# Kernel optimization log

Hardware: AMD Instinct MI355X
Metric: run time of the kernel (lower is better)

Reference implementation:

```python
import jax, jax.numpy as jnp
import numpy as np

K = 8        # fused SOS sections
C = 64       # channels (B*C after reshape)
T = 262144   # time samples (~6 s @ 44.1 kHz)


def setup_inputs() -> dict:
    key = jax.random.key(0)
    kx, kb, ka1, ka2 = jax.random.split(key, 4)
    x = jax.random.normal(kx, (C, T), dtype=jnp.float32)
    # Stable biquad coefficients: a0 = 1, |a1| < 0.5, |a2| < 0.4 keeps poles
    # strictly inside the unit circle (|a1| < 1 + a2 and |a2| < 1).
    b = jax.random.normal(kb, (K, 3), dtype=jnp.float32) * 0.3
    a1 = jax.random.uniform(ka1, (K, 1), minval=-0.5, maxval=0.5, dtype=jnp.float32)
    a2 = jax.random.uniform(ka2, (K, 1), minval=-0.4, maxval=0.4, dtype=jnp.float32)
    sos = jnp.concatenate([b, jnp.ones((K, 1), jnp.float32), a1, a2], axis=1)
    state_x = jnp.zeros((K, C, 2), jnp.float32)  # [x[n-1], x[n-2]] per section/channel
    state_y = jnp.zeros((K, C, 2), jnp.float32)  # [y[n-1], y[n-2]]
    return {"x": x, "sos": sos, "state_x": state_x, "state_y": state_y}


def _biquad_df1(x, b0, b1, b2, a1, a2, sx, sy):
    """Direct-form-1 biquad over time, vectorized across channels.

    x: [C, T]; sx, sy: [C, 2] holding (lag1, lag2). Returns y: [C, T].
    """
    def step(carry, xn):
        x1, x2, y1, y2 = carry
        yn = b0 * xn + b1 * x1 + b2 * x2 - a1 * y1 - a2 * y2
        return (xn, x1, yn, y1), yn

    init = (sx[:, 0], sx[:, 1], sy[:, 0], sy[:, 1])
    _, ys = jax.lax.scan(step, init, x.T)  # scan over T, carry [C]
    return ys.T


def reference(x, sos, state_x, state_y):
    # Serial cascade of K second-order sections (fallback path of forward()).
    out = x
    k = sos.shape[0]
    for s in range(k):
        out = _biquad_df1(out, sos[s, 0], sos[s, 1], sos[s, 2],
                          sos[s, 4], sos[s, 5], state_x[s], state_y[s])
    return out
```

## Files before the change

kernel.cpp:

```cpp
#include <hip/hip_runtime.h>

#define C 64
#define T 262144
#define K 8
#define L 128
#define W 192
#define B (T / L)
#define TT 64
#define STRIDE 65

__device__ __forceinline__ void async_ld(const float* gp, float* ldsbase) {
  __builtin_amdgcn_global_load_lds(
      (const __attribute__((address_space(1))) void*)gp,
      (__attribute__((address_space(3))) void*)ldsbase, 4, 0, 0);
}

#define STEP(Y1, Y2, U1, U2, XIN)                                            \
  {                                                                          \
    float tkv[K];                                                            \
    tkv[0] = fmaf(b1c[0], U1,                                                \
             fmaf(b2c[0], U2, fmaf(na1[0], Y1[0], na2[0] * Y2[0])));         \
    _Pragma("unroll")                                                        \
    for (int k = 1; k < K; ++k)                                              \
      tkv[k] = fmaf(b1c[k], Y1[k - 1],                                       \
               fmaf(b2c[k], Y2[k - 1],                                       \
               fmaf(na1[k], Y1[k], na2[k] * Y2[k])));                        \
    float o = fmaf(b0c[0], (XIN), tkv[0]);                                   \
    U2 = (XIN);                                                              \
    _Pragma("unroll")                                                        \
    for (int k = 1; k < K; ++k) {                                            \
      float o2 = fmaf(b0c[k], o, tkv[k]);                                    \
      Y2[k - 1] = o;                                                         \
      o = o2;                                                                \
    }                                                                        \
    Y2[K - 1] = o;                                                           \
    lastout = o;                                                             \
  }

__global__ __launch_bounds__(64) void sos_kernel(
    const float* __restrict__ x, const float* __restrict__ sos,
    const float* __restrict__ sx, const float* __restrict__ sy,
    float* __restrict__ out) {
  __shared__ float lbuf[64 * STRIDE];

  const int h = blockIdx.x;
  const int b = (h & 7) * (B / 8) + (h >> 3);
  const int lane = threadIdx.x;

  float b0c[K], b1c[K], b2c[K], na1[K], na2[K];
#pragma unroll
  for (int k = 0; k < K; ++k) {
    b0c[k] = sos[k * 6 + 0];
    b1c[k] = sos[k * 6 + 1];
    b2c[k] = sos[k * 6 + 2];
    na1[k] = -sos[k * 6 + 4];
    na2[k] = -sos[k * 6 + 5];
  }

  const int t_out = b * L;
  const int tstart = (t_out >= W) ? (t_out - W) : 0;
  const int nch = (t_out + L - tstart) / TT;

  float yA[K], yB[K], uA, uB;
  if (tstart == 0) {
    uA = sx[lane * 2 + 0];
    uB = sx[lane * 2 + 1];
#pragma unroll
    for (int k = 0; k < K; ++k) {
      yA[k] = sy[(k * 64 + lane) * 2 + 0];
      yB[k] = sy[(k * 64 + lane) * 2 + 1];
    }
  } else {
    uA = x[(size_t)lane * T + tstart - 1];
    uB = x[(size_t)lane * T + tstart - 2];
#pragma unroll
    for (int k = 0; k < K; ++k) { yA[k] = 0.f; yB[k] = 0.f; }
  }

  float lastout = 0.f;
  for (int ch = 0; ch < nch; ++ch) {
    const int tc = tstart + ch * TT;
    __syncthreads();
#pragma unroll
    for (int r = 0; r < 64; ++r)
      async_ld(x + (size_t)r * T + tc + lane, &lbuf[r * STRIDE]);
    __syncthreads();

    float* myrow = &lbuf[lane * STRIDE];

    float xg0[8], xg1[8];
#pragma unroll
    for (int j = 0; j < 8; ++j) xg0[j] = myrow[j];
    for (int gg = 0; gg < TT / 16; ++gg) {
      const int tb = gg * 16;
#pragma unroll
      for (int j = 0; j < 8; ++j) xg1[j] = myrow[tb + 8 + j];
#pragma unroll
      for (int j = 0; j < 8; j += 2) {
        STEP(yA, yB, uA, uB, xg0[j])
        myrow[tb + j] = lastout;
        STEP(yB, yA, uB, uA, xg0[j + 1])
        myrow[tb + j + 1] = lastout;
      }
      if (gg + 1 < TT / 16) {
#pragma unroll
        for (int j = 0; j < 8; ++j) xg0[j] = myrow[tb + 16 + j];
      }
#pragma unroll
      for (int j = 0; j < 8; j += 2) {
        STEP(yA, yB, uA, uB, xg1[j])
        myrow[tb + 8 + j] = lastout;
        STEP(yB, yA, uB, uA, xg1[j + 1])
        myrow[tb + 8 + j + 1] = lastout;
      }
    }

    if (tc >= t_out) {
      __syncthreads();
#pragma unroll 8
      for (int r = 0; r < 64; ++r)
        out[(size_t)r * T + tc + lane] = lbuf[r * STRIDE + lane];
    }
  }
  (void)lastout;
}

extern "C" void kernel_launch(void* const* d_in, const int* in_sizes, int n_in,
                              void* d_out, int out_size, void* d_ws,
                              size_t ws_size, hipStream_t stream) {
  const float* x = (const float*)d_in[0];
  const float* sos = (const float*)d_in[1];
  const float* sx = (const float*)d_in[2];
  const float* sy = (const float*)d_in[3];
  float* out = (float*)d_out;
  (void)d_ws;

  sos_kernel<<<B, 64, 0, stream>>>(x, sos, sx, sy, out);
}
```

Measured before the change: 160.6 us.

## Prefetch next chunk into registers during compute and vectorize output stores

Replaces the direct global-to-LDS async loads with register staging: each lane loads the next 64-sample chunk into a 64-float register array while the current chunk is filtered, then writes it into LDS after the compute. The aim is to hide global load latency behind the recurrence instead of stalling at a barrier before each chunk. Output stores become float4 writes over a remapped lane/row layout, and launch bounds ask for 2 blocks per CU. The 64-register staging buffer adds register pressure, which may cause spills or lower occupancy.

```diff
diff --git a/kernel.cpp b/kernel.cpp
--- a/kernel.cpp
+++ b/kernel.cpp
@@ -8,12 +8,6 @@
 #define B (T / L)
 #define TT 64
 #define STRIDE 65
-
-__device__ __forceinline__ void async_ld(const float* gp, float* ldsbase) {
-  __builtin_amdgcn_global_load_lds(
-      (const __attribute__((address_space(1))) void*)gp,
-      (__attribute__((address_space(3))) void*)ldsbase, 4, 0, 0);
-}
 
 #define STEP(Y1, Y2, U1, U2, XIN)                                            \
   {                                                                          \
@@ -37,7 +31,7 @@
     lastout = o;                                                             \
   }
 
-__global__ __launch_bounds__(64) void sos_kernel(
+__global__ __launch_bounds__(64, 2) void sos_kernel(
     const float* __restrict__ x, const float* __restrict__ sos,
     const float* __restrict__ sx, const float* __restrict__ sy,
     float* __restrict__ out) {
@@ -77,14 +71,23 @@
     for (int k = 0; k < K; ++k) { yA[k] = 0.f; yB[k] = 0.f; }
   }
 
+  float st[64];
+
+#pragma unroll
+  for (int r = 0; r < 64; ++r) st[r] = x[(size_t)r * T + tstart + lane];
+#pragma unroll
+  for (int r = 0; r < 64; ++r) lbuf[r * STRIDE + lane] = st[r];
+  __syncthreads();
+
   float lastout = 0.f;
   for (int ch = 0; ch < nch; ++ch) {
     const int tc = tstart + ch * TT;
-    __syncthreads();
+
+    if (ch + 1 < nch) {
+      const int tn = tc + TT;
 #pragma unroll
-    for (int r = 0; r < 64; ++r)
-      async_ld(x + (size_t)r * T + tc + lane, &lbuf[r * STRIDE]);
-    __syncthreads();
+      for (int r = 0; r < 64; ++r) st[r] = x[(size_t)r * T + tn + lane];
+    }
 
     float* myrow = &lbuf[lane * STRIDE];
 
@@ -115,11 +118,28 @@
       }
     }
 
+    __syncthreads();
+
     if (tc >= t_out) {
+      const int rr = lane >> 4;
+      const int cc = (lane & 15) * 4;
+#pragma unroll
+      for (int it = 0; it < 16; ++it) {
+        const int r = it * 4 + rr;
+        float4 v;
+        v.x = lbuf[r * STRIDE + cc + 0];
+        v.y = lbuf[r * STRIDE + cc + 1];
+        v.z = lbuf[r * STRIDE + cc + 2];
+        v.w = lbuf[r * STRIDE + cc + 3];
+        *reinterpret_cast<float4*>(&out[(size_t)r * T + tc + cc]) = v;
+      }
+      if (ch + 1 < nch) __syncthreads();
+    }
+
+    if (ch + 1 < nch) {
+#pragma unroll
+      for (int r = 0; r < 64; ++r) lbuf[r * STRIDE + lane] = st[r];
       __syncthreads();
-#pragma unroll 8
-      for (int r = 0; r < 64; ++r)
-        out[(size_t)r * T + tc + lane] = lbuf[r * STRIDE + lane];
     }
   }
   (void)lastout;
```

Result: no change. 159.6 us (-0.6%).

## Load input straight into registers with prefetch instead of LDS staging

Applied to the files above, without the earlier changes.

Drops the per-chunk async global-to-LDS transpose of the input, along with its two barriers. Each lane now reads its own channel row as float4 vectors into two 16-element register buffers, and the next group is prefetched while the current one is filtered. Output is still staged through LDS, but it is written to global memory with coalesced float4 stores, and the launch bound now requests two blocks per SIMD. In exchange, the per-lane global loads are strided across rows, register pressure goes up, and the barrier before the output transpose is gone, which relies on the block being a single wavefront.

```diff
diff --git a/kernel.cpp b/kernel.cpp
--- a/kernel.cpp
+++ b/kernel.cpp
@@ -7,13 +7,8 @@
 #define W 192
 #define B (T / L)
 #define TT 64
-#define STRIDE 65
-
-__device__ __forceinline__ void async_ld(const float* gp, float* ldsbase) {
-  __builtin_amdgcn_global_load_lds(
-      (const __attribute__((address_space(1))) void*)gp,
-      (__attribute__((address_space(3))) void*)ldsbase, 4, 0, 0);
-}
+#define OSTRIDE 65
+#define TMAX (T - 16)
 
 #define STEP(Y1, Y2, U1, U2, XIN)                                            \
   {                                                                          \
@@ -37,11 +32,30 @@
     lastout = o;                                                             \
   }
 
-__global__ __launch_bounds__(64) void sos_kernel(
+#define GROUP(XS, CBASE)                                                     \
+  _Pragma("unroll")                                                          \
+  for (int j = 0; j < 16; j += 2) {                                          \
+    STEP(yA, yB, uA, uB, XS[j])                                              \
+    orow[(CBASE) + j] = lastout;                                             \
+    STEP(yB, yA, uB, uA, XS[j + 1])                                          \
+    orow[(CBASE) + j + 1] = lastout;                                         \
+  }
+
+#define LOAD16(DST, PTR)                                                     \
+  {                                                                          \
+    const float4* p4_ = (const float4*)(PTR);                                \
+    float4 q0_ = p4_[0], q1_ = p4_[1], q2_ = p4_[2], q3_ = p4_[3];           \
+    DST[0] = q0_.x;  DST[1] = q0_.y;  DST[2] = q0_.z;  DST[3] = q0_.w;       \
+    DST[4] = q1_.x;  DST[5] = q1_.y;  DST[6] = q1_.z;  DST[7] = q1_.w;       \
+    DST[8] = q2_.x;  DST[9] = q2_.y;  DST[10] = q2_.z; DST[11] = q2_.w;      \
+    DST[12] = q3_.x; DST[13] = q3_.y; DST[14] = q3_.z; DST[15] = q3_.w;      \
+  }
+
+__global__ __launch_bounds__(64, 2) void sos_kernel(
     const float* __restrict__ x, const float* __restrict__ sos,
     const float* __restrict__ sx, const float* __restrict__ sy,
     float* __restrict__ out) {
-  __shared__ float lbuf[64 * STRIDE];
+  __shared__ float obuf[64 * OSTRIDE];
 
   const int h = blockIdx.x;
   const int b = (h & 7) * (B / 8) + (h >> 3);
@@ -61,6 +75,9 @@
   const int tstart = (t_out >= W) ? (t_out - W) : 0;
   const int nch = (t_out + L - tstart) / TT;
 
+  const float* xrow = x + (size_t)lane * T;
+  float* orow = &obuf[lane * OSTRIDE];
+
   float yA[K], yB[K], uA, uB;
   if (tstart == 0) {
     uA = sx[lane * 2 + 0];
@@ -71,55 +88,44 @@
       yB[k] = sy[(k * 64 + lane) * 2 + 1];
     }
   } else {
-    uA = x[(size_t)lane * T + tstart - 1];
-    uB = x[(size_t)lane * T + tstart - 2];
+    uA = xrow[tstart - 1];
+    uB = xrow[tstart - 2];
 #pragma unroll
     for (int k = 0; k < K; ++k) { yA[k] = 0.f; yB[k] = 0.f; }
   }
 
+  float xA[16], xB[16];
+  LOAD16(xA, xrow + tstart)
+  LOAD16(xB, xrow + tstart + 16)
+
   float lastout = 0.f;
   for (int ch = 0; ch < nch; ++ch) {
     const int tc = tstart + ch * TT;
-    __syncthreads();
-#pragma unroll
-    for (int r = 0; r < 64; ++r)
-      async_ld(x + (size_t)r * T + tc + lane, &lbuf[r * STRIDE]);
-    __syncthreads();
 
-    float* myrow = &lbuf[lane * STRIDE];
-
-    float xg0[8], xg1[8];
-#pragma unroll
-    for (int j = 0; j < 8; ++j) xg0[j] = myrow[j];
-    for (int gg = 0; gg < TT / 16; ++gg) {
-      const int tb = gg * 16;
-#pragma unroll
-      for (int j = 0; j < 8; ++j) xg1[j] = myrow[tb + 8 + j];
-#pragma unroll
-      for (int j = 0; j < 8; j += 2) {
-        STEP(yA, yB, uA, uB, xg0[j])
-        myrow[tb + j] = lastout;
-        STEP(yB, yA, uB, uA, xg0[j + 1])
-        myrow[tb + j + 1] = lastout;
-      }
-      if (gg + 1 < TT / 16) {
-#pragma unroll
-        for (int j = 0; j < 8; ++j) xg0[j] = myrow[tb + 16 + j];
-      }
-#pragma unroll
-      for (int j = 0; j < 8; j += 2) {
-        STEP(yA, yB, uA, uB, xg1[j])
-        myrow[tb + 8 + j] = lastout;
-        STEP(yB, yA, uB, uA, xg1[j + 1])
-        myrow[tb + 8 + j + 1] = lastout;
-      }
-    }
+    GROUP(xA, 0)
+    { int tl = tc + 32;  LOAD16(xA, xrow + tl) }
+    GROUP(xB, 16)
+    { int tl = tc + 48;  LOAD16(xB, xrow + tl) }
+    GROUP(xA, 32)
+    { int tl = tc + 64;  if (tl > TMAX) tl = TMAX;
+      LOAD16(xA, xrow + tl) }
+    GROUP(xB, 48)
+    { int tl = tc + 80;  if (tl > TMAX) tl = TMAX;
+      LOAD16(xB, xrow + tl) }
 
     if (tc >= t_out) {
-      __syncthreads();
-#pragma unroll 8
-      for (int r = 0; r < 64; ++r)
-        out[(size_t)r * T + tc + lane] = lbuf[r * STRIDE + lane];
+      const int rr = lane >> 4;
+      const int cc = (lane & 15) * 4;
+#pragma unroll
+      for (int it = 0; it < 16; ++it) {
+        const int r = it * 4 + rr;
+        float4 v;
+        v.x = obuf[r * OSTRIDE + cc + 0];
+        v.y = obuf[r * OSTRIDE + cc + 1];
+        v.z = obuf[r * OSTRIDE + cc + 2];
+        v.w = obuf[r * OSTRIDE + cc + 3];
+        *reinterpret_cast<float4*>(&out[(size_t)r * T + tc + cc]) = v;
+      }
     }
   }
   (void)lastout;
```

New measurement: 153.4 us. -4.5%, faster.
